# Performance work log

Measured on AMD Instinct MI355X. Metric: run time of the kernel, lower is better.

## Reference

```python
import jax, jax.numpy as jnp
import numpy as np

ALPHA = 1.0 / 50.0  # dt / tau with dt=1, tau=50

T, B, I, H = 1024, 64, 128, 512


def setup_inputs() -> dict:
    key = jax.random.key(0)
    k1, k2, k3, k4 = jax.random.split(key, 4)
    x = jax.random.normal(k1, (T, B, I), dtype=jnp.float32)
    # input2h.weight ~ N(0, 0.5^2), shape [H, I]
    W_in = 0.5 * jax.random.normal(k2, (H, I), dtype=jnp.float32)
    # h2h.weight ~ N(0, 1/sqrt(H)^2), shape [H, H]
    W_h = jax.random.normal(k3, (H, H), dtype=jnp.float32) / np.sqrt(H).astype(np.float32)
    # initial_hidden ~ U(-1, 1), shape [1, H]
    h0 = jax.random.uniform(k4, (1, H), dtype=jnp.float32) * 2.0 - 1.0
    return {"x": x, "W_in": W_in, "W_h": W_h, "h0": h0}


def reference(x, W_in, W_h, h0):
    # Precompute input projection for all timesteps in one big GEMM:
    # [T, B, I] @ [I, H] -> [T, B, H]
    x_proj = jnp.einsum('tbi,hi->tbh', x, W_in)
    hidden0 = jnp.broadcast_to(h0, (x.shape[1], h0.shape[1]))  # [B, H]

    def step(hidden, xp_t):
        h_new = jax.nn.sigmoid(xp_t + hidden @ W_h.T)
        h_new = hidden * (1.0 - ALPHA) + h_new * ALPHA
        return h_new, h_new

    hidden_final, output = jax.lax.scan(step, hidden0, x_proj)
    return output, hidden_final
```

## Files before the change

kernel.cpp:

```cpp
#include <hip/hip_runtime.h>

#define T_STEPS 1024
#define BATCH   64
#define IDIM    128
#define HDIM    512
#define ALPHA_F 0.02f

typedef _Float16 half2_t __attribute__((ext_vector_type(2)));
typedef unsigned int uint32;

__device__ __forceinline__ float dot2f(uint32 w, uint32 h, float acc) {
#if __has_builtin(__builtin_amdgcn_fdot2)
  return __builtin_amdgcn_fdot2(__builtin_bit_cast(half2_t, w),
                                __builtin_bit_cast(half2_t, h), acc, false);
#else
  half2_t a = __builtin_bit_cast(half2_t, w);
  half2_t b = __builtin_bit_cast(half2_t, h);
  return acc + (float)a.x * (float)b.x + (float)a.y * (float)b.y;
#endif
}

__device__ __forceinline__ uint32 pk2(float a, float b) {
  auto p = __builtin_amdgcn_cvt_pkrtz(a, b);
  return __builtin_bit_cast(uint32, p);
}

__device__ __forceinline__ int dot4i8(uint32 a, uint32 b, int c) {
#if __has_builtin(__builtin_amdgcn_sdot4)
  return __builtin_amdgcn_sdot4((int)a, (int)b, c, false);
#else
  int s = c;
  s += (int)(signed char)(a)        * (int)(signed char)(b);
  s += (int)(signed char)(a >> 8)   * (int)(signed char)(b >> 8);
  s += (int)(signed char)(a >> 16)  * (int)(signed char)(b >> 16);
  s += (int)(signed char)(a >> 24)  * (int)(signed char)(b >> 24);
  return s;
#endif
}

__device__ __forceinline__ uint32 pkq(float v0, float v1, float v2, float v3, float inv) {
  int i0 = __float2int_rn(v0 * inv), i1 = __float2int_rn(v1 * inv);
  int i2 = __float2int_rn(v2 * inv), i3 = __float2int_rn(v3 * inv);
  return (uint32)(i0 & 255) | ((uint32)(i1 & 255) << 8) |
         ((uint32)(i2 & 255) << 16) | ((uint32)(i3 & 255) << 24);
}

__device__ __forceinline__ int dpp_xor1(int x) {
#if __has_builtin(__builtin_amdgcn_mov_dpp)
  return __builtin_amdgcn_mov_dpp(x, 0xB1, 0xF, 0xF, true);
#else
  return __shfl_xor(x, 1);
#endif
}
__device__ __forceinline__ int dpp_xor2(int x) {
#if __has_builtin(__builtin_amdgcn_mov_dpp)
  return __builtin_amdgcn_mov_dpp(x, 0x4E, 0xF, 0xF, true);
#else
  return __shfl_xor(x, 2);
#endif
}
__device__ __forceinline__ int swz_xor4(int x) {
#if __has_builtin(__builtin_amdgcn_ds_swizzle)
  return __builtin_amdgcn_ds_swizzle(x, 0x101F);
#else
  return __shfl_xor(x, 4);
#endif
}
__device__ __forceinline__ float fxor1(float x) {
  return __builtin_bit_cast(float, dpp_xor1(__builtin_bit_cast(int, x)));
}
__device__ __forceinline__ float fxor2(float x) {
  return __builtin_bit_cast(float, dpp_xor2(__builtin_bit_cast(int, x)));
}
__device__ __forceinline__ float fxor4(float x) {
  return __builtin_bit_cast(float, swz_xor4(__builtin_bit_cast(int, x)));
}

__global__ __launch_bounds__(512) void ctrnn_proj(
    const float* __restrict__ x,
    const float* __restrict__ Win,
    float* __restrict__ xp,
    int rows) {
  const int j = threadIdx.x;
  __shared__ __attribute__((aligned(16))) uint32 xb[8][64];

  uint32 w[64];
  const float2* wr = (const float2*)(Win + (size_t)j * IDIM);
#pragma unroll
  for (int p = 0; p < 64; ++p) {
    float2 f = wr[p];
    w[p] = pk2(f.x, f.y);
  }

  const int m0 = blockIdx.x * 128;
  for (int it = 0; it < 16; ++it) {
    const int mb = m0 + it * 8;
    __syncthreads();
    if (j < 256) {
      const int r = j >> 5, q = j & 31;
      const int m = mb + r;
      float4 v = make_float4(0.f, 0.f, 0.f, 0.f);
      if (m < rows) v = *(const float4*)(x + (size_t)m * IDIM + q * 4);
      xb[r][2 * q]     = pk2(v.x, v.y);
      xb[r][2 * q + 1] = pk2(v.z, v.w);
    }
    __syncthreads();
#pragma unroll
    for (int r = 0; r < 8; ++r) {
      const int m = mb + r;
      if (m < rows) {
        const uint4* xv = (const uint4*)xb[r];
        float a0 = 0.f, a1 = 0.f, a2 = 0.f, a3 = 0.f;
#pragma unroll
        for (int c = 0; c < 16; ++c) {
          uint4 hx = xv[c];
          a0 = dot2f(w[4 * c + 0], hx.x, a0);
          a1 = dot2f(w[4 * c + 1], hx.y, a1);
          a2 = dot2f(w[4 * c + 2], hx.z, a2);
          a3 = dot2f(w[4 * c + 3], hx.w, a3);
        }
        xp[(size_t)m * HDIM + j] = (a0 + a1) + (a2 + a3);
      }
    }
  }
}

__global__ __launch_bounds__(512)
__attribute__((amdgpu_waves_per_eu(2, 2)))
void ctrnn_scan(
    const float* __restrict__ xp,
    const float* __restrict__ Wh,
    const float* __restrict__ h0,
    float* __restrict__ out,
    int t0, int ct) {
  const int b = blockIdx.x;
  const int j = threadIdx.x;
  const int g = j & 7;
  const int o = j >> 3;

  __shared__ __attribute__((aligned(16))) unsigned char hq[2][640];

  float m[8];
#pragma unroll
  for (int i = 0; i < 8; ++i) {
    const float4* wr = (const float4*)(Wh + (size_t)(8 * o + (i ^ g)) * HDIM + 64 * g);
    float mm = 0.f;
#pragma unroll
    for (int c = 0; c < 16; ++c) {
      float4 v = wr[c];
      mm = fmaxf(mm, fmaxf(fmaxf(fabsf(v.x), fabsf(v.y)), fmaxf(fabsf(v.z), fabsf(v.w))));
    }
    m[i] = mm;
  }
  {
    float t[8];
#pragma unroll
    for (int i = 0; i < 8; ++i) t[i] = fmaxf(m[i], fxor1(m[i ^ 1]));
#pragma unroll
    for (int i = 0; i < 8; ++i) m[i] = fmaxf(t[i], fxor2(t[i ^ 2]));
#pragma unroll
    for (int i = 0; i < 8; ++i) t[i] = fmaxf(m[i], fxor4(m[i ^ 4]));
#pragma unroll
    for (int i = 0; i < 8; ++i) m[i] = t[i];
  }

  uint32 w[128];
#pragma unroll
  for (int i = 0; i < 8; ++i) {
    const float rm = m[i];
    const float inv = (rm > 0.f) ? 127.f / rm : 0.f;
    const float4* wr = (const float4*)(Wh + (size_t)(8 * o + (i ^ g)) * HDIM + 64 * g);
#pragma unroll
    for (int c = 0; c < 16; ++c) {
      float4 v = wr[c];
      w[i * 16 + c] = pkq(v.x, v.y, v.z, v.w, inv);
    }
  }
  const float fscale = m[0] * (1.f / (127.f * 127.f));

  float h;
  if (t0 == 0) h = h0[j];
  else h = out[((size_t)(t0 - 1) * BATCH + b) * HDIM + j];
  {
    uint32 bb = (uint32)(__float2int_rn(h * 127.f) & 255);
    uint32 c1 = bb | ((uint32)dpp_xor1((int)bb) << 8);
    uint32 dw = c1 | ((uint32)dpp_xor2((int)c1) << 16);
    if ((j & 3) == 0) *((uint32*)&hq[0][j + 16 * (j >> 6)]) = dw;
  }
  __syncthreads();

  const float* xpp = xp + (size_t)b * HDIM + j;
  float* outp = out + ((size_t)t0 * BATCH + b) * HDIM + j;
  const size_t BH = (size_t)BATCH * HDIM;

  float xp_cur = xpp[0];
  int cur = 0;
  for (int t = 0; t < ct; ++t) {
    const float xp_nxt = xpp[(t + 1 < ct) ? BH : 0];

    const uint4* hb = (const uint4*)(&hq[cur][80 * g]);
    int a0 = 0, a1 = 0, a2 = 0, a3 = 0, a4 = 0, a5 = 0, a6 = 0, a7 = 0;
#pragma unroll
    for (int c = 0; c < 4; ++c) {
      uint4 hv = hb[c];
      a0 = dot4i8(w[0 * 16 + 4 * c + 0], hv.x, a0);
      a0 = dot4i8(w[0 * 16 + 4 * c + 1], hv.y, a0);
      a0 = dot4i8(w[0 * 16 + 4 * c + 2], hv.z, a0);
      a0 = dot4i8(w[0 * 16 + 4 * c + 3], hv.w, a0);
      a1 = dot4i8(w[1 * 16 + 4 * c + 0], hv.x, a1);
      a1 = dot4i8(w[1 * 16 + 4 * c + 1], hv.y, a1);
      a1 = dot4i8(w[1 * 16 + 4 * c + 2], hv.z, a1);
      a1 = dot4i8(w[1 * 16 + 4 * c + 3], hv.w, a1);
      a2 = dot4i8(w[2 * 16 + 4 * c + 0], hv.x, a2);
      a2 = dot4i8(w[2 * 16 + 4 * c + 1], hv.y, a2);
      a2 = dot4i8(w[2 * 16 + 4 * c + 2], hv.z, a2);
      a2 = dot4i8(w[2 * 16 + 4 * c + 3], hv.w, a2);
      a3 = dot4i8(w[3 * 16 + 4 * c + 0], hv.x, a3);
      a3 = dot4i8(w[3 * 16 + 4 * c + 1], hv.y, a3);
      a3 = dot4i8(w[3 * 16 + 4 * c + 2], hv.z, a3);
      a3 = dot4i8(w[3 * 16 + 4 * c + 3], hv.w, a3);
      a4 = dot4i8(w[4 * 16 + 4 * c + 0], hv.x, a4);
      a4 = dot4i8(w[4 * 16 + 4 * c + 1], hv.y, a4);
      a4 = dot4i8(w[4 * 16 + 4 * c + 2], hv.z, a4);
      a4 = dot4i8(w[4 * 16 + 4 * c + 3], hv.w, a4);
      a5 = dot4i8(w[5 * 16 + 4 * c + 0], hv.x, a5);
      a5 = dot4i8(w[5 * 16 + 4 * c + 1], hv.y, a5);
      a5 = dot4i8(w[5 * 16 + 4 * c + 2], hv.z, a5);
      a5 = dot4i8(w[5 * 16 + 4 * c + 3], hv.w, a5);
      a6 = dot4i8(w[6 * 16 + 4 * c + 0], hv.x, a6);
      a6 = dot4i8(w[6 * 16 + 4 * c + 1], hv.y, a6);
      a6 = dot4i8(w[6 * 16 + 4 * c + 2], hv.z, a6);
      a6 = dot4i8(w[6 * 16 + 4 * c + 3], hv.w, a6);
      a7 = dot4i8(w[7 * 16 + 4 * c + 0], hv.x, a7);
      a7 = dot4i8(w[7 * 16 + 4 * c + 1], hv.y, a7);
      a7 = dot4i8(w[7 * 16 + 4 * c + 2], hv.z, a7);
      a7 = dot4i8(w[7 * 16 + 4 * c + 3], hv.w, a7);
    }
    const int q0 = a0 + dpp_xor1(a1);
    const int q1 = a2 + dpp_xor1(a3);
    const int q2 = a4 + dpp_xor1(a5);
    const int q3 = a6 + dpp_xor1(a7);
    const int r0 = q0 + dpp_xor2(q1);
    const int r1 = q2 + dpp_xor2(q3);
    const int res = r0 + swz_xor4(r1);

    const float z = (float)res * fscale + xp_cur;
    const float s = 1.0f / (1.0f + __expf(-z));
    h = h * (1.0f - ALPHA_F) + s * ALPHA_F;

    *outp = h;

    uint32 bb = (uint32)(__float2int_rn(h * 127.f) & 255);
    uint32 c1 = bb | ((uint32)dpp_xor1((int)bb) << 8);
    uint32 dw = c1 | ((uint32)dpp_xor2((int)c1) << 16);
    if ((j & 3) == 0) *((uint32*)&hq[cur ^ 1][j + 16 * (j >> 6)]) = dw;
    __syncthreads();
    cur ^= 1;
    xp_cur = xp_nxt;
    xpp += BH;
    outp += BH;
  }

  if (t0 + ct == T_STEPS) {
    out[(size_t)T_STEPS * BATCH * HDIM + (size_t)b * HDIM + j] = h;
  }
}

extern "C" void kernel_launch(void* const* d_in, const int* in_sizes, int n_in,
                              void* d_out, int out_size, void* d_ws, size_t ws_size,
                              hipStream_t stream) {
  const float* x   = (const float*)d_in[0];
  const float* Win = (const float*)d_in[1];
  const float* Wh  = (const float*)d_in[2];
  const float* h0  = (const float*)d_in[3];
  float* out = (float*)d_out;
  float* xp  = (float*)d_ws;

  const size_t step_bytes = (size_t)BATCH * HDIM * sizeof(float);
  int ct_max = (int)(ws_size / step_bytes);
  if (ct_max < 1) ct_max = 1;
  if (ct_max > T_STEPS) ct_max = T_STEPS;

  for (int t0 = 0; t0 < T_STEPS; t0 += ct_max) {
    const int ct = (T_STEPS - t0 < ct_max) ? (T_STEPS - t0) : ct_max;
    const int rows = ct * BATCH;
    const int nb = (rows + 127) / 128;
    hipLaunchKernelGGL(ctrnn_proj, dim3(nb), dim3(512), 0, stream,
                       x + (size_t)t0 * BATCH * IDIM, Win, xp, rows);
    hipLaunchKernelGGL(ctrnn_scan, dim3(BATCH), dim3(512), 0, stream,
                       xp, Wh, h0, out, t0, ct);
  }
}
```

Measured before the change: 931.2 us.

## Halve scan block size so each thread computes two hidden units

The recurrent scan kernel now runs 256 threads per batch row instead of 512, and each thread owns two output neurons with 256 int8-packed weight registers instead of 128. The goal is fewer waves synchronizing at each per-timestep barrier and more independent dot-product chains per thread to hide latency. In exchange, register pressure doubles to one wave per EU, and per-step serial work per thread roughly doubles, which may lengthen the critical path of the recurrence.

```diff
diff --git a/kernel.cpp b/kernel.cpp
--- a/kernel.cpp
+++ b/kernel.cpp
@@ -125,8 +125,10 @@
   }
 }
 
-__global__ __launch_bounds__(512)
-__attribute__((amdgpu_waves_per_eu(2, 2)))
+__device__ __forceinline__ int h_byte(int r) { return 80 * (r >> 6) + (r & 63); }
+
+__global__ __launch_bounds__(256)
+__attribute__((amdgpu_waves_per_eu(1, 1)))
 void ctrnn_scan(
     const float* __restrict__ xp,
     const float* __restrict__ Wh,
@@ -137,13 +139,16 @@
   const int j = threadIdx.x;
   const int g = j & 7;
   const int o = j >> 3;
+  const int n1 = 16 * o + g;
+  const int n2 = n1 + 8;
 
   __shared__ __attribute__((aligned(16))) unsigned char hq[2][640];
 
-  float m[8];
-#pragma unroll
-  for (int i = 0; i < 8; ++i) {
-    const float4* wr = (const float4*)(Wh + (size_t)(8 * o + (i ^ g)) * HDIM + 64 * g);
+  float m[16];
+#pragma unroll
+  for (int i = 0; i < 16; ++i) {
+    const int row = 16 * o + 8 * (i >> 3) + ((i & 7) ^ g);
+    const float4* wr = (const float4*)(Wh + (size_t)row * HDIM + 64 * g);
     float mm = 0.f;
 #pragma unroll
     for (int c = 0; c < 16; ++c) {
@@ -153,116 +158,133 @@
     m[i] = mm;
   }
   {
-    float t[8];
-#pragma unroll
-    for (int i = 0; i < 8; ++i) t[i] = fmaxf(m[i], fxor1(m[i ^ 1]));
-#pragma unroll
-    for (int i = 0; i < 8; ++i) m[i] = fmaxf(t[i], fxor2(t[i ^ 2]));
-#pragma unroll
-    for (int i = 0; i < 8; ++i) t[i] = fmaxf(m[i], fxor4(m[i ^ 4]));
-#pragma unroll
-    for (int i = 0; i < 8; ++i) m[i] = t[i];
-  }
-
-  uint32 w[128];
-#pragma unroll
-  for (int i = 0; i < 8; ++i) {
+    float t[16];
+#pragma unroll
+    for (int i = 0; i < 16; ++i) t[i] = fmaxf(m[i], fxor1(m[i ^ 1]));
+#pragma unroll
+    for (int i = 0; i < 16; ++i) m[i] = fmaxf(t[i], fxor2(t[i ^ 2]));
+#pragma unroll
+    for (int i = 0; i < 16; ++i) t[i] = fmaxf(m[i], fxor4(m[i ^ 4]));
+#pragma unroll
+    for (int i = 0; i < 16; ++i) m[i] = t[i];
+  }
+
+  uint32 w[256];
+#pragma unroll
+  for (int i = 0; i < 16; ++i) {
     const float rm = m[i];
     const float inv = (rm > 0.f) ? 127.f / rm : 0.f;
-    const float4* wr = (const float4*)(Wh + (size_t)(8 * o + (i ^ g)) * HDIM + 64 * g);
+    const int row = 16 * o + 8 * (i >> 3) + ((i & 7) ^ g);
+    const float4* wr = (const float4*)(Wh + (size_t)row * HDIM + 64 * g);
 #pragma unroll
     for (int c = 0; c < 16; ++c) {
       float4 v = wr[c];
       w[i * 16 + c] = pkq(v.x, v.y, v.z, v.w, inv);
     }
   }
-  const float fscale = m[0] * (1.f / (127.f * 127.f));
-
-  float h;
-  if (t0 == 0) h = h0[j];
-  else h = out[((size_t)(t0 - 1) * BATCH + b) * HDIM + j];
+  const float fscale1 = m[0] * (1.f / (127.f * 127.f));
+  const float fscale2 = m[8] * (1.f / (127.f * 127.f));
+
+  float h1, h2;
+  if (t0 == 0) { h1 = h0[n1]; h2 = h0[n2]; }
+  else {
+    const float* prev = out + ((size_t)(t0 - 1) * BATCH + b) * HDIM;
+    h1 = prev[n1]; h2 = prev[n2];
+  }
   {
-    uint32 bb = (uint32)(__float2int_rn(h * 127.f) & 255);
-    uint32 c1 = bb | ((uint32)dpp_xor1((int)bb) << 8);
-    uint32 dw = c1 | ((uint32)dpp_xor2((int)c1) << 16);
-    if ((j & 3) == 0) *((uint32*)&hq[0][j + 16 * (j >> 6)]) = dw;
+    uint32 bA = (uint32)(__float2int_rn(h1 * 127.f) & 255);
+    uint32 cA = bA | ((uint32)dpp_xor1((int)bA) << 8);
+    uint32 dA = cA | ((uint32)dpp_xor2((int)cA) << 16);
+    uint32 bB = (uint32)(__float2int_rn(h2 * 127.f) & 255);
+    uint32 cB = bB | ((uint32)dpp_xor1((int)bB) << 8);
+    uint32 dB = cB | ((uint32)dpp_xor2((int)cB) << 16);
+    if (g == 0) {
+      *((uint32*)&hq[0][h_byte(16 * o)])     = dA;
+      *((uint32*)&hq[0][h_byte(16 * o + 8)]) = dB;
+    } else if (g == 4) {
+      *((uint32*)&hq[0][h_byte(16 * o + 4)])  = dA;
+      *((uint32*)&hq[0][h_byte(16 * o + 12)]) = dB;
+    }
   }
   __syncthreads();
 
-  const float* xpp = xp + (size_t)b * HDIM + j;
-  float* outp = out + ((size_t)t0 * BATCH + b) * HDIM + j;
+  const float* xpp1 = xp + (size_t)b * HDIM + n1;
+  const float* xpp2 = xp + (size_t)b * HDIM + n2;
+  float* outp1 = out + ((size_t)t0 * BATCH + b) * HDIM + n1;
+  float* outp2 = out + ((size_t)t0 * BATCH + b) * HDIM + n2;
   const size_t BH = (size_t)BATCH * HDIM;
 
-  float xp_cur = xpp[0];
+  float xp1 = xpp1[0], xp2 = xpp2[0];
   int cur = 0;
   for (int t = 0; t < ct; ++t) {
-    const float xp_nxt = xpp[(t + 1 < ct) ? BH : 0];
+    const size_t pre = (t + 1 < ct) ? BH : 0;
+    const float xp1n = xpp1[pre];
+    const float xp2n = xpp2[pre];
 
     const uint4* hb = (const uint4*)(&hq[cur][80 * g]);
-    int a0 = 0, a1 = 0, a2 = 0, a3 = 0, a4 = 0, a5 = 0, a6 = 0, a7 = 0;
+    int a[16];
+#pragma unroll
+    for (int i = 0; i < 16; ++i) a[i] = 0;
 #pragma unroll
     for (int c = 0; c < 4; ++c) {
       uint4 hv = hb[c];
-      a0 = dot4i8(w[0 * 16 + 4 * c + 0], hv.x, a0);
-      a0 = dot4i8(w[0 * 16 + 4 * c + 1], hv.y, a0);
-      a0 = dot4i8(w[0 * 16 + 4 * c + 2], hv.z, a0);
-      a0 = dot4i8(w[0 * 16 + 4 * c + 3], hv.w, a0);
-      a1 = dot4i8(w[1 * 16 + 4 * c + 0], hv.x, a1);
-      a1 = dot4i8(w[1 * 16 + 4 * c + 1], hv.y, a1);
-      a1 = dot4i8(w[1 * 16 + 4 * c + 2], hv.z, a1);
-      a1 = dot4i8(w[1 * 16 + 4 * c + 3], hv.w, a1);
-      a2 = dot4i8(w[2 * 16 + 4 * c + 0], hv.x, a2);
-      a2 = dot4i8(w[2 * 16 + 4 * c + 1], hv.y, a2);
-      a2 = dot4i8(w[2 * 16 + 4 * c + 2], hv.z, a2);
-      a2 = dot4i8(w[2 * 16 + 4 * c + 3], hv.w, a2);
-      a3 = dot4i8(w[3 * 16 + 4 * c + 0], hv.x, a3);
-      a3 = dot4i8(w[3 * 16 + 4 * c + 1], hv.y, a3);
-      a3 = dot4i8(w[3 * 16 + 4 * c + 2], hv.z, a3);
-      a3 = dot4i8(w[3 * 16 + 4 * c + 3], hv.w, a3);
-      a4 = dot4i8(w[4 * 16 + 4 * c + 0], hv.x, a4);
-      a4 = dot4i8(w[4 * 16 + 4 * c + 1], hv.y, a4);
-      a4 = dot4i8(w[4 * 16 + 4 * c + 2], hv.z, a4);
-      a4 = dot4i8(w[4 * 16 + 4 * c + 3], hv.w, a4);
-      a5 = dot4i8(w[5 * 16 + 4 * c + 0], hv.x, a5);
-      a5 = dot4i8(w[5 * 16 + 4 * c + 1], hv.y, a5);
-      a5 = dot4i8(w[5 * 16 + 4 * c + 2], hv.z, a5);
-      a5 = dot4i8(w[5 * 16 + 4 * c + 3], hv.w, a5);
-      a6 = dot4i8(w[6 * 16 + 4 * c + 0], hv.x, a6);
-      a6 = dot4i8(w[6 * 16 + 4 * c + 1], hv.y, a6);
-      a6 = dot4i8(w[6 * 16 + 4 * c + 2], hv.z, a6);
-      a6 = dot4i8(w[6 * 16 + 4 * c + 3], hv.w, a6);
-      a7 = dot4i8(w[7 * 16 + 4 * c + 0], hv.x, a7);
-      a7 = dot4i8(w[7 * 16 + 4 * c + 1], hv.y, a7);
-      a7 = dot4i8(w[7 * 16 + 4 * c + 2], hv.z, a7);
-      a7 = dot4i8(w[7 * 16 + 4 * c + 3], hv.w, a7);
-    }
-    const int q0 = a0 + dpp_xor1(a1);
-    const int q1 = a2 + dpp_xor1(a3);
-    const int q2 = a4 + dpp_xor1(a5);
-    const int q3 = a6 + dpp_xor1(a7);
-    const int r0 = q0 + dpp_xor2(q1);
-    const int r1 = q2 + dpp_xor2(q3);
-    const int res = r0 + swz_xor4(r1);
-
-    const float z = (float)res * fscale + xp_cur;
-    const float s = 1.0f / (1.0f + __expf(-z));
-    h = h * (1.0f - ALPHA_F) + s * ALPHA_F;
-
-    *outp = h;
-
-    uint32 bb = (uint32)(__float2int_rn(h * 127.f) & 255);
-    uint32 c1 = bb | ((uint32)dpp_xor1((int)bb) << 8);
-    uint32 dw = c1 | ((uint32)dpp_xor2((int)c1) << 16);
-    if ((j & 3) == 0) *((uint32*)&hq[cur ^ 1][j + 16 * (j >> 6)]) = dw;
+#pragma unroll
+      for (int i = 0; i < 16; ++i) {
+        a[i] = dot4i8(w[i * 16 + 4 * c + 0], hv.x, a[i]);
+        a[i] = dot4i8(w[i * 16 + 4 * c + 1], hv.y, a[i]);
+        a[i] = dot4i8(w[i * 16 + 4 * c + 2], hv.z, a[i]);
+        a[i] = dot4i8(w[i * 16 + 4 * c + 3], hv.w, a[i]);
+      }
+    }
+    const int q0  = a[0]  + dpp_xor1(a[1]);
+    const int q2  = a[2]  + dpp_xor1(a[3]);
+    const int q4  = a[4]  + dpp_xor1(a[5]);
+    const int q6  = a[6]  + dpp_xor1(a[7]);
+    const int q8  = a[8]  + dpp_xor1(a[9]);
+    const int q10 = a[10] + dpp_xor1(a[11]);
+    const int q12 = a[12] + dpp_xor1(a[13]);
+    const int q14 = a[14] + dpp_xor1(a[15]);
+    const int r0  = q0  + dpp_xor2(q2);
+    const int r4  = q4  + dpp_xor2(q6);
+    const int r8  = q8  + dpp_xor2(q10);
+    const int r12 = q12 + dpp_xor2(q14);
+    const int s0  = r0  + swz_xor4(r4);
+    const int s8  = r8  + swz_xor4(r12);
+
+    const float z1 = (float)s0 * fscale1 + xp1;
+    const float z2 = (float)s8 * fscale2 + xp2;
+    const float sg1 = 1.0f / (1.0f + __expf(-z1));
+    const float sg2 = 1.0f / (1.0f + __expf(-z2));
+    h1 = h1 * (1.0f - ALPHA_F) + sg1 * ALPHA_F;
+    h2 = h2 * (1.0f - ALPHA_F) + sg2 * ALPHA_F;
+
+    *outp1 = h1;
+    *outp2 = h2;
+
+    uint32 bA = (uint32)(__float2int_rn(h1 * 127.f) & 255);
+    uint32 cA = bA | ((uint32)dpp_xor1((int)bA) << 8);
+    uint32 dA = cA | ((uint32)dpp_xor2((int)cA) << 16);
+    uint32 bB = (uint32)(__float2int_rn(h2 * 127.f) & 255);
+    uint32 cB = bB | ((uint32)dpp_xor1((int)bB) << 8);
+    uint32 dB = cB | ((uint32)dpp_xor2((int)cB) << 16);
+    if (g == 0) {
+      *((uint32*)&hq[cur ^ 1][h_byte(16 * o)])     = dA;
+      *((uint32*)&hq[cur ^ 1][h_byte(16 * o + 8)]) = dB;
+    } else if (g == 4) {
+      *((uint32*)&hq[cur ^ 1][h_byte(16 * o + 4)])  = dA;
+      *((uint32*)&hq[cur ^ 1][h_byte(16 * o + 12)]) = dB;
+    }
     __syncthreads();
     cur ^= 1;
-    xp_cur = xp_nxt;
-    xpp += BH;
-    outp += BH;
+    xp1 = xp1n; xp2 = xp2n;
+    xpp1 += BH; xpp2 += BH;
+    outp1 += BH; outp2 += BH;
   }
 
   if (t0 + ct == T_STEPS) {
-    out[(size_t)T_STEPS * BATCH * HDIM + (size_t)b * HDIM + j] = h;
+    float* fin = out + (size_t)T_STEPS * BATCH * HDIM + (size_t)b * HDIM;
+    fin[n1] = h1;
+    fin[n2] = h2;
   }
 }
 
@@ -287,7 +309,7 @@
     const int nb = (rows + 127) / 128;
     hipLaunchKernelGGL(ctrnn_proj, dim3(nb), dim3(512), 0, stream,
                        x + (size_t)t0 * BATCH * IDIM, Win, xp, rows);
-    hipLaunchKernelGGL(ctrnn_scan, dim3(BATCH), dim3(512), 0, stream,
+    hipLaunchKernelGGL(ctrnn_scan, dim3(BATCH), dim3(256), 0, stream,
                        xp, Wh, h0, out, t0, ct);
   }
 }
```

After: 1.172 ms. 25.8% more time.

## Move a quarter of int8 recurrent weights from registers into LDS

Applied to the files above, without the earlier changes.

Each thread now keeps 96 of its 128 packed int8 weight words in VGPRs and stores the other 32 in a 64 KB shared-memory array, reading them back as uint4 loads interleaved with the register-resident dot products. This is meant to relieve register pressure, and with it spills or scheduling limits, in the per-timestep recurrent matvec. The cost is extra LDS traffic every step. The software prefetch of the next timestep's input projection is also removed, so that global load is now exposed on the critical path each step.

```diff
diff --git a/kernel.cpp b/kernel.cpp
--- a/kernel.cpp
+++ b/kernel.cpp
@@ -124,6 +124,26 @@
     }
   }
 }
+
+#define REGD(acc, i)                                  \
+  acc = dot4i8(w[(i)*12 + 0], hv0.x, acc);            \
+  acc = dot4i8(w[(i)*12 + 1], hv0.y, acc);            \
+  acc = dot4i8(w[(i)*12 + 2], hv0.z, acc);            \
+  acc = dot4i8(w[(i)*12 + 3], hv0.w, acc);            \
+  acc = dot4i8(w[(i)*12 + 4], hv1.x, acc);            \
+  acc = dot4i8(w[(i)*12 + 5], hv1.y, acc);            \
+  acc = dot4i8(w[(i)*12 + 6], hv1.z, acc);            \
+  acc = dot4i8(w[(i)*12 + 7], hv1.w, acc);            \
+  acc = dot4i8(w[(i)*12 + 8], hv2.x, acc);            \
+  acc = dot4i8(w[(i)*12 + 9], hv2.y, acc);            \
+  acc = dot4i8(w[(i)*12 +10], hv2.z, acc);            \
+  acc = dot4i8(w[(i)*12 +11], hv2.w, acc);
+
+#define LDSD(acc, wv)                                 \
+  acc = dot4i8(wv.x, hv3.x, acc);                     \
+  acc = dot4i8(wv.y, hv3.y, acc);                     \
+  acc = dot4i8(wv.z, hv3.z, acc);                     \
+  acc = dot4i8(wv.w, hv3.w, acc);
 
 __global__ __launch_bounds__(512)
 __attribute__((amdgpu_waves_per_eu(2, 2)))
@@ -138,6 +158,7 @@
   const int g = j & 7;
   const int o = j >> 3;
 
+  __shared__ __attribute__((aligned(16))) uint4 wl[8][512];
   __shared__ __attribute__((aligned(16))) unsigned char hq[2][640];
 
   float m[8];
@@ -164,17 +185,22 @@
     for (int i = 0; i < 8; ++i) m[i] = t[i];
   }
 
-  uint32 w[128];
+  uint32 w[96];
 #pragma unroll
   for (int i = 0; i < 8; ++i) {
     const float rm = m[i];
     const float inv = (rm > 0.f) ? 127.f / rm : 0.f;
     const float4* wr = (const float4*)(Wh + (size_t)(8 * o + (i ^ g)) * HDIM + 64 * g);
 #pragma unroll
-    for (int c = 0; c < 16; ++c) {
+    for (int c = 0; c < 12; ++c) {
       float4 v = wr[c];
-      w[i * 16 + c] = pkq(v.x, v.y, v.z, v.w, inv);
-    }
+      w[i * 12 + c] = pkq(v.x, v.y, v.z, v.w, inv);
+    }
+    float4 vA = wr[12], vB = wr[13], vC = wr[14], vD = wr[15];
+    wl[i][j] = make_uint4(pkq(vA.x, vA.y, vA.z, vA.w, inv),
+                          pkq(vB.x, vB.y, vB.z, vB.w, inv),
+                          pkq(vC.x, vC.y, vC.z, vC.w, inv),
+                          pkq(vD.x, vD.y, vD.z, vD.w, inv));
   }
   const float fscale = m[0] * (1.f / (127.f * 127.f));
 
@@ -193,49 +219,25 @@
   float* outp = out + ((size_t)t0 * BATCH + b) * HDIM + j;
   const size_t BH = (size_t)BATCH * HDIM;
 
-  float xp_cur = xpp[0];
   int cur = 0;
   for (int t = 0; t < ct; ++t) {
-    const float xp_nxt = xpp[(t + 1 < ct) ? BH : 0];
+    const float xp_c = *xpp;
 
     const uint4* hb = (const uint4*)(&hq[cur][80 * g]);
+    const uint4 hv0 = hb[0], hv1 = hb[1], hv2 = hb[2], hv3 = hb[3];
+
+    uint4 wvA = wl[0][j];
+    uint4 wvB = wl[1][j];
     int a0 = 0, a1 = 0, a2 = 0, a3 = 0, a4 = 0, a5 = 0, a6 = 0, a7 = 0;
-#pragma unroll
-    for (int c = 0; c < 4; ++c) {
-      uint4 hv = hb[c];
-      a0 = dot4i8(w[0 * 16 + 4 * c + 0], hv.x, a0);
-      a0 = dot4i8(w[0 * 16 + 4 * c + 1], hv.y, a0);
-      a0 = dot4i8(w[0 * 16 + 4 * c + 2], hv.z, a0);
-      a0 = dot4i8(w[0 * 16 + 4 * c + 3], hv.w, a0);
-      a1 = dot4i8(w[1 * 16 + 4 * c + 0], hv.x, a1);
-      a1 = dot4i8(w[1 * 16 + 4 * c + 1], hv.y, a1);
-      a1 = dot4i8(w[1 * 16 + 4 * c + 2], hv.z, a1);
-      a1 = dot4i8(w[1 * 16 + 4 * c + 3], hv.w, a1);
-      a2 = dot4i8(w[2 * 16 + 4 * c + 0], hv.x, a2);
-      a2 = dot4i8(w[2 * 16 + 4 * c + 1], hv.y, a2);
-      a2 = dot4i8(w[2 * 16 + 4 * c + 2], hv.z, a2);
-      a2 = dot4i8(w[2 * 16 + 4 * c + 3], hv.w, a2);
-      a3 = dot4i8(w[3 * 16 + 4 * c + 0], hv.x, a3);
-      a3 = dot4i8(w[3 * 16 + 4 * c + 1], hv.y, a3);
-      a3 = dot4i8(w[3 * 16 + 4 * c + 2], hv.z, a3);
-      a3 = dot4i8(w[3 * 16 + 4 * c + 3], hv.w, a3);
-      a4 = dot4i8(w[4 * 16 + 4 * c + 0], hv.x, a4);
-      a4 = dot4i8(w[4 * 16 + 4 * c + 1], hv.y, a4);
-      a4 = dot4i8(w[4 * 16 + 4 * c + 2], hv.z, a4);
-      a4 = dot4i8(w[4 * 16 + 4 * c + 3], hv.w, a4);
-      a5 = dot4i8(w[5 * 16 + 4 * c + 0], hv.x, a5);
-      a5 = dot4i8(w[5 * 16 + 4 * c + 1], hv.y, a5);
-      a5 = dot4i8(w[5 * 16 + 4 * c + 2], hv.z, a5);
-      a5 = dot4i8(w[5 * 16 + 4 * c + 3], hv.w, a5);
-      a6 = dot4i8(w[6 * 16 + 4 * c + 0], hv.x, a6);
-      a6 = dot4i8(w[6 * 16 + 4 * c + 1], hv.y, a6);
-      a6 = dot4i8(w[6 * 16 + 4 * c + 2], hv.z, a6);
-      a6 = dot4i8(w[6 * 16 + 4 * c + 3], hv.w, a6);
-      a7 = dot4i8(w[7 * 16 + 4 * c + 0], hv.x, a7);
-      a7 = dot4i8(w[7 * 16 + 4 * c + 1], hv.y, a7);
-      a7 = dot4i8(w[7 * 16 + 4 * c + 2], hv.z, a7);
-      a7 = dot4i8(w[7 * 16 + 4 * c + 3], hv.w, a7);
-    }
+    REGD(a0, 0) LDSD(a0, wvA) wvA = wl[2][j];
+    REGD(a1, 1) LDSD(a1, wvB) wvB = wl[3][j];
+    REGD(a2, 2) LDSD(a2, wvA) wvA = wl[4][j];
+    REGD(a3, 3) LDSD(a3, wvB) wvB = wl[5][j];
+    REGD(a4, 4) LDSD(a4, wvA) wvA = wl[6][j];
+    REGD(a5, 5) LDSD(a5, wvB) wvB = wl[7][j];
+    REGD(a6, 6) LDSD(a6, wvA)
+    REGD(a7, 7) LDSD(a7, wvB)
+
     const int q0 = a0 + dpp_xor1(a1);
     const int q1 = a2 + dpp_xor1(a3);
     const int q2 = a4 + dpp_xor1(a5);
@@ -244,7 +246,7 @@
     const int r1 = q2 + dpp_xor2(q3);
     const int res = r0 + swz_xor4(r1);
 
-    const float z = (float)res * fscale + xp_cur;
+    const float z = (float)res * fscale + xp_c;
     const float s = 1.0f / (1.0f + __expf(-z));
     h = h * (1.0f - ALPHA_F) + s * ALPHA_F;
 
@@ -256,7 +258,6 @@
     if ((j & 3) == 0) *((uint32*)&hq[cur ^ 1][j + 16 * (j >> 6)]) = dw;
     __syncthreads();
     cur ^= 1;
-    xp_cur = xp_nxt;
     xpp += BH;
     outp += BH;
   }
```

Result: slower. 1.128 ms (+21.1%).
